# Performance work log

Measured on AMD Instinct MI355X. Metric: run time of the kernel, lower is better.

The kernel has to match this reference:

```python
import jax, jax.numpy as jnp
import numpy as np
import math

B, M, N = 1, 128, 256
LIG_C = 256      # rep_1d num_c
ATTN_C = 32      # attention_num_c
HEADS = 8        # num_heads
EPS = 1e-5


def setup_inputs() -> dict:
    key = jax.random.key(0)
    ks = jax.random.split(key, 8)
    s = 1.0 / math.sqrt(LIG_C)
    return {
        "lig_profile": jax.random.normal(ks[0], (B, M, N, LIG_C), dtype=jnp.float32),
        "ln_scale": jnp.ones((LIG_C,), dtype=jnp.float32),
        "ln_bias": jnp.zeros((LIG_C,), dtype=jnp.float32),
        "wq": jax.random.normal(ks[1], (LIG_C, ATTN_C * HEADS), dtype=jnp.float32) * s,
        "wk": jax.random.normal(ks[2], (LIG_C, ATTN_C * HEADS), dtype=jnp.float32) * s,
        "wv": jax.random.normal(ks[3], (LIG_C, ATTN_C * HEADS), dtype=jnp.float32) * s,
        "wf": jax.random.normal(ks[4], (ATTN_C * HEADS, LIG_C), dtype=jnp.float32) * s,
        "bf": jnp.zeros((LIG_C,), dtype=jnp.float32),
    }


def reference(lig_profile, ln_scale, ln_bias, wq, wk, wv, wf, bf):
    # LayerNorm over channel dim
    mu = jnp.mean(lig_profile, axis=-1, keepdims=True)
    var = jnp.mean(jnp.square(lig_profile - mu), axis=-1, keepdims=True)
    x = (lig_profile - mu) * jax.lax.rsqrt(var + EPS) * ln_scale + ln_bias

    # QKV projections; view splits last dim as (attn_c, heads) -> channel-major layout
    shape5 = x.shape[:-1] + (ATTN_C, HEADS)
    q = (x @ wq).reshape(shape5)  # [b,m,n,c,h]
    k = (x @ wk).reshape(shape5)
    v = (x @ wv).reshape(shape5)

    factor = 1.0 / math.sqrt(ATTN_C)
    aff = jnp.einsum('bmich,bmjch->bmijh', q, k) * factor  # [b,m,i,j,h]
    weights = jax.nn.softmax(aff, axis=-2)                  # softmax over j (keys)
    out = jnp.einsum('bmrch,bmirh->bmich', v, weights)      # [b,m,i,c,h]
    out = out.reshape(out.shape[:-2] + (ATTN_C * HEADS,))
    return out @ wf + bf
```

## Files before the change

kernel.cpp:

```cpp
#include <hip/hip_runtime.h>

typedef _Float16 f16;
typedef _Float16 f16x8 __attribute__((ext_vector_type(8)));
typedef _Float16 f16x4 __attribute__((ext_vector_type(4)));
typedef _Float16 f16x2 __attribute__((ext_vector_type(2)));
typedef float f32x4 __attribute__((ext_vector_type(4)));
typedef float f32x16 __attribute__((ext_vector_type(16)));

#define MDIM 128
#define NDIM 256
#define CDIM 256
#define ROWS (MDIM*NDIM)
#define L2E 1.4426950408889634f

__device__ inline int pk2(float a, float b) {
  union { f16x2 h; int i; } u;
  u.h[0] = (f16)a; u.h[1] = (f16)b;
  return u.i;
}

__global__ __launch_bounds__(256) void k_prep(
    const float* __restrict__ wq, const float* __restrict__ wk,
    const float* __restrict__ wv, const float* __restrict__ wf,
    f16* __restrict__ bq, f16* __restrict__ bk, f16* __restrict__ bv,
    f16* __restrict__ bw)
{
  __shared__ f16 ld[16][264];
  int which = blockIdx.x >> 4, kb = blockIdx.x & 15;
  int t = threadIdx.x;
  int k0 = kb * 16;
  if (which < 3) {
    const float* W = which == 0 ? wq : which == 1 ? wk : wv;
    f16* dst       = which == 0 ? bq : which == 1 ? bk : bv;
    float sc = which == 0 ? 0.17677669529663689f : 1.0f;
#pragma unroll
    for (int r = 0; r < 16; ++r)
      ld[r][t] = (f16)(W[(size_t)(k0 + r) * 256 + t] * sc);
    __syncthreads();
    int j = (t & 31) * 8 + (t >> 5);
    f16x8 o;
#pragma unroll
    for (int i = 0; i < 8; ++i) o[i] = ld[i][j];
    *(f16x8*)(dst + (size_t)t * 256 + k0) = o;
#pragma unroll
    for (int i = 0; i < 8; ++i) o[i] = ld[8 + i][j];
    *(f16x8*)(dst + (size_t)t * 256 + k0 + 8) = o;
  } else {
#pragma unroll
    for (int r = 0; r < 16; ++r) {
      int ke = k0 + r;
      int jr = (ke & 31) * 8 + (ke >> 5);
      ld[r][t] = (f16)wf[(size_t)jr * 256 + t];
    }
    __syncthreads();
    f16x8 o;
#pragma unroll
    for (int i = 0; i < 8; ++i) o[i] = ld[i][t];
    *(f16x8*)(bw + (size_t)t * 256 + k0) = o;
#pragma unroll
    for (int i = 0; i < 8; ++i) o[i] = ld[8 + i][t];
    *(f16x8*)(bw + (size_t)t * 256 + k0 + 8) = o;
  }
}

__global__ __launch_bounds__(256) void k_ln(const float* __restrict__ x,
                                            const float* __restrict__ g,
                                            const float* __restrict__ b,
                                            f16* __restrict__ y)
{
  int row  = blockIdx.x * 4 + (threadIdx.x >> 6);
  int lane = threadIdx.x & 63;
  const float4 xv = *(const float4*)(x + (size_t)row * CDIM + lane * 4);
  float s  = xv.x + xv.y + xv.z + xv.w;
  float s2 = xv.x*xv.x + xv.y*xv.y + xv.z*xv.z + xv.w*xv.w;
#pragma unroll
  for (int m = 1; m < 64; m <<= 1) {
    s  += __shfl_xor(s,  m, 64);
    s2 += __shfl_xor(s2, m, 64);
  }
  float mu  = s * (1.0f / CDIM);
  float var = s2 * (1.0f / CDIM) - mu * mu;
  float rs  = rsqrtf(var + 1e-5f);
  const float4 gv = *(const float4*)(g + lane * 4);
  const float4 bv = *(const float4*)(b + lane * 4);
  f16x4 o;
  o[0] = (f16)((xv.x - mu) * rs * gv.x + bv.x);
  o[1] = (f16)((xv.y - mu) * rs * gv.y + bv.y);
  o[2] = (f16)((xv.z - mu) * rs * gv.z + bv.z);
  o[3] = (f16)((xv.w - mu) * rs * gv.w + bv.w);
  *(f16x4*)(y + (size_t)row * CDIM + lane * 4) = o;
}

__global__ __launch_bounds__(256) void k_qkv(const f16* __restrict__ xh,
    const f16* __restrict__ bq, const f16* __restrict__ bk, const f16* __restrict__ bv,
    f16* __restrict__ qo, f16* __restrict__ ko, f16* __restrict__ vT)
{
  __shared__ f16 Bs[64][264];
  __shared__ f16 vtmp[4][64][18];
  int mp = blockIdx.x;
  int nc = blockIdx.y;
  int sec = nc >> 2;
  int c0  = (nc & 3) * 64;
  const f16* B = sec == 0 ? bq : sec == 1 ? bk : bv;
  f16* dst     = sec == 0 ? qo : ko;
  int t = threadIdx.x, lane = t & 63, w = t >> 6;
  int l15 = lane & 15, l4 = lane >> 4;
  {
    int pr = t >> 2, pc = (t & 3) * 8;
#pragma unroll
    for (int p = 0; p < 8; ++p)
      *(f16x8*)&Bs[pr][pc + p * 32] =
        *(const f16x8*)(B + (size_t)(c0 + pr) * 256 + pc + p * 32);
  }
  __syncthreads();
  for (int it = 0; it < 4; ++it) {
    int r0 = mp * 256 + it * 64 + w * 16;
    f16x8 af[8];
#pragma unroll
    for (int kt = 0; kt < 8; ++kt)
      af[kt] = *(const f16x8*)(xh + (size_t)(r0 + l15) * 256 + kt * 32 + l4 * 8);
    f32x4 acc[4] = {};
#pragma unroll
    for (int kt = 0; kt < 8; ++kt) {
#pragma unroll
      for (int ni = 0; ni < 4; ++ni) {
        f16x8 bf = *(const f16x8*)&Bs[ni * 16 + l15][kt * 32 + l4 * 8];
        acc[ni] = __builtin_amdgcn_mfma_f32_16x16x32_f16(af[kt], bf, acc[ni], 0, 0, 0);
      }
    }
    if (sec < 2) {
#pragma unroll
      for (int ni = 0; ni < 4; ++ni)
#pragma unroll
        for (int r = 0; r < 4; ++r)
          dst[(size_t)(r0 + l4 * 4 + r) * 256 + c0 + ni * 16 + l15] = (f16)acc[ni][r];
    } else {
#pragma unroll
      for (int ni = 0; ni < 4; ++ni)
#pragma unroll
        for (int r = 0; r < 4; ++r)
          vtmp[w][ni * 16 + l15][l4 * 4 + r] = (f16)acc[ni][r];
      int n0 = it * 64 + w * 16;
      f16x8 v0 = *(const f16x8*)&vtmp[w][lane][0];
      f16x8 v1 = *(const f16x8*)&vtmp[w][lane][8];
      size_t gd = ((size_t)mp * 256 + c0 + lane) * 256 + n0;
      *(f16x8*)(vT + gd)     = v0;
      *(f16x8*)(vT + gd + 8) = v1;
    }
  }
}

__global__ __launch_bounds__(512, 4) void k_attn(const f16* __restrict__ q,
    const f16* __restrict__ k, const f16* __restrict__ vT, f16* __restrict__ o)
{
  __shared__ f16 ks[256][40];
  __shared__ f16 vt[32][264];
  int bx = blockIdx.x;
  int m = bx >> 3, h = bx & 7;
  int t = threadIdx.x, lane = t & 63, w = t >> 6;
  int i32 = lane & 31, hi = lane >> 5;
  size_t rowbase = (size_t)m * 256;
#pragma unroll
  for (int p = 0; p < 2; ++p) {
    int n = p * 128 + (t >> 2);
    int c0 = (t & 3) * 8;
    *(f16x8*)&ks[n][c0] = *(const f16x8*)(k + (rowbase + n) * 256 + h * 32 + c0);
  }
#pragma unroll
  for (int p = 0; p < 2; ++p) {
    int idx = p * 512 + t;
    int c = idx >> 5, nb = (idx & 31) * 8;
    *(f16x8*)&vt[c][nb] = *(const f16x8*)(vT + ((size_t)m * 256 + h * 32 + c) * 256 + nb);
  }
  __syncthreads();
  int qi0 = w * 32;
  const f16* qp = q + (rowbase + qi0 + i32) * 256 + h * 32 + hi * 8;
  f16x8 qf0 = *(const f16x8*)(qp);
  f16x8 qf1 = *(const f16x8*)(qp + 16);
  f32x16 O = {};
  float m_run = -1e30f, l_run = 0.f;
#pragma unroll 2
  for (int kb = 0; kb < 8; ++kb) {
    f16x8 kf0 = *(const f16x8*)&ks[kb * 32 + i32][hi * 8];
    f16x8 kf1 = *(const f16x8*)&ks[kb * 32 + i32][16 + hi * 8];
    f32x16 s = {};
    __builtin_amdgcn_s_setprio(1);
    s = __builtin_amdgcn_mfma_f32_32x32x16_f16(kf0, qf0, s, 0, 0, 0);
    s = __builtin_amdgcn_mfma_f32_32x32x16_f16(kf1, qf1, s, 0, 0, 0);
    __builtin_amdgcn_s_setprio(0);
#pragma unroll
    for (int r = 0; r < 16; ++r) s[r] *= L2E;
    float pmax = s[0];
#pragma unroll
    for (int r = 1; r < 16; ++r) pmax = fmaxf(pmax, s[r]);
    pmax = fmaxf(pmax, __shfl_xor(pmax, 32, 64));
    if (!__all(pmax - m_run <= 8.f)) {
      float m_new = fmaxf(m_run, pmax);
      float f = __builtin_amdgcn_exp2f(m_run - m_new);
      l_run *= f;
#pragma unroll
      for (int r = 0; r < 16; ++r)
        O[r] *= __shfl(f, (r & 3) + 8 * (r >> 2) + 4 * hi, 64);
      m_run = m_new;
    }
    float lsum = 0.f;
#pragma unroll
    for (int r = 0; r < 16; ++r) {
      float e = __builtin_amdgcn_exp2f(s[r] - m_run);
      s[r] = e;
      lsum += e;
    }
    lsum += __shfl_xor(lsum, 32, 64);
    l_run += lsum;
    int W0[4], W1[4];
#pragma unroll
    for (int qq = 0; qq < 4; ++qq) {
      W0[qq] = pk2(s[4 * qq],     s[4 * qq + 1]);
      W1[qq] = pk2(s[4 * qq + 2], s[4 * qq + 3]);
    }
#pragma unroll
    for (int ks2 = 0; ks2 < 2; ++ks2) {
      int X0 = W0[2 * ks2], Y0 = W0[2 * ks2 + 1];
      int X1 = W1[2 * ks2], Y1 = W1[2 * ks2 + 1];
      int a0 = __shfl(X0, i32, 64),      b0 = __shfl(Y0, i32, 64);
      int a1 = __shfl(X1, i32, 64),      b1 = __shfl(Y1, i32, 64);
      int a2 = __shfl(X0, i32 + 32, 64), b2 = __shfl(Y0, i32 + 32, 64);
      int a3 = __shfl(X1, i32 + 32, 64), b3 = __shfl(Y1, i32 + 32, 64);
      union { unsigned int ww[4]; f16x8 v; } pa;
      pa.ww[0] = hi ? (unsigned)b0 : (unsigned)a0;
      pa.ww[1] = hi ? (unsigned)b1 : (unsigned)a1;
      pa.ww[2] = hi ? (unsigned)b2 : (unsigned)a2;
      pa.ww[3] = hi ? (unsigned)b3 : (unsigned)a3;
      f16x8 vb = *(const f16x8*)&vt[i32][kb * 32 + ks2 * 16 + hi * 8];
      __builtin_amdgcn_s_setprio(1);
      O = __builtin_amdgcn_mfma_f32_32x32x16_f16(pa.v, vb, O, 0, 0, 0);
      __builtin_amdgcn_s_setprio(0);
    }
  }
  float inv = 1.f / l_run;
#pragma unroll
  for (int r = 0; r < 16; ++r) {
    int i = (r & 3) + 8 * (r >> 2) + 4 * hi;
    float fr = __shfl(inv, i, 64);
    o[(rowbase + (size_t)(qi0 + i)) * 256 + h * 32 + i32] = (f16)(O[r] * fr);
  }
}

__global__ __launch_bounds__(256) void k_out(const f16* __restrict__ a,
    const f16* __restrict__ bw, const float* __restrict__ bias,
    float* __restrict__ out)
{
  __shared__ f16 Bs[64][264];
  int mp = blockIdx.x;
  int nc = blockIdx.y;
  int c0 = nc * 64;
  int t = threadIdx.x, lane = t & 63, w = t >> 6;
  int l15 = lane & 15, l4 = lane >> 4;
  {
    int pr = t >> 2, pc = (t & 3) * 8;
#pragma unroll
    for (int p = 0; p < 8; ++p)
      *(f16x8*)&Bs[pr][pc + p * 32] =
        *(const f16x8*)(bw + (size_t)(c0 + pr) * 256 + pc + p * 32);
  }
  __syncthreads();
  float bv[4];
#pragma unroll
  for (int ni = 0; ni < 4; ++ni) bv[ni] = bias[c0 + ni * 16 + l15];
  for (int it = 0; it < 4; ++it) {
    int r0 = mp * 256 + it * 64 + w * 16;
    f16x8 af[8];
#pragma unroll
    for (int kt = 0; kt < 8; ++kt)
      af[kt] = *(const f16x8*)(a + (size_t)(r0 + l15) * 256 + kt * 32 + l4 * 8);
    f32x4 acc[4] = {};
#pragma unroll
    for (int kt = 0; kt < 8; ++kt) {
#pragma unroll
      for (int ni = 0; ni < 4; ++ni) {
        f16x8 bf = *(const f16x8*)&Bs[ni * 16 + l15][kt * 32 + l4 * 8];
        acc[ni] = __builtin_amdgcn_mfma_f32_16x16x32_f16(af[kt], bf, acc[ni], 0, 0, 0);
      }
    }
#pragma unroll
    for (int ni = 0; ni < 4; ++ni)
#pragma unroll
      for (int r = 0; r < 4; ++r)
        out[(size_t)(r0 + l4 * 4 + r) * 256 + c0 + ni * 16 + l15] = acc[ni][r] + bv[ni];
  }
}

extern "C" void kernel_launch(void* const* d_in, const int* in_sizes, int n_in,
                              void* d_out, int out_size, void* d_ws, size_t ws_size,
                              hipStream_t stream)
{
  const float* x  = (const float*)d_in[0];
  const float* g  = (const float*)d_in[1];
  const float* b  = (const float*)d_in[2];
  const float* wq = (const float*)d_in[3];
  const float* wk = (const float*)d_in[4];
  const float* wv = (const float*)d_in[5];
  const float* wf = (const float*)d_in[6];
  const float* bf = (const float*)d_in[7];
  float* out = (float*)d_out;

  char* ws = (char*)d_ws;
  f16* xh  = (f16*)(ws);
  f16* qh  = (f16*)(ws + (size_t)16 * 1024 * 1024);
  f16* kh  = (f16*)(ws + (size_t)32 * 1024 * 1024);
  f16* vTh = (f16*)(ws + (size_t)48 * 1024 * 1024);
  char* wbase = ws + (size_t)64 * 1024 * 1024;
  f16* bq = (f16*)(wbase);
  f16* bk = (f16*)(wbase + 128 * 1024);
  f16* bv = (f16*)(wbase + 256 * 1024);
  f16* bw = (f16*)(wbase + 384 * 1024);
  f16* ah = (f16*)(ws + (size_t)80 * 1024 * 1024);

  k_prep<<<64,            256, 0, stream>>>(wq, wk, wv, wf, bq, bk, bv, bw);
  k_ln  <<<ROWS / 4,      256, 0, stream>>>(x, g, b, xh);
  k_qkv <<<dim3(128, 12), 256, 0, stream>>>(xh, bq, bk, bv, qh, kh, vTh);
  k_attn<<<1024,          512, 0, stream>>>(qh, kh, vTh, ah);
  k_out <<<dim3(128, 4),  256, 0, stream>>>(ah, bw, bf, out);
}
```

Baseline: 95.07 us.

## Widen QKV tiles, drop V transpose, fold log2e into exp, retile output GEMM

The QKV GEMM now computes 128 output columns per block (6 column groups instead of 12) and writes V row-major, so the separate LDS transpose staging for V goes away. The attention kernel transposes V into shared memory itself with scalar LDS stores. It also folds the log2(e) scale into an FMA inside the exp and rescales the lazy-rescale threshold to match. The output GEMM is retiled so each block keeps a 64-row A tile in LDS and loops over four 64-column weight tiles, prefetching the next one into registers. The cost is scalar transposed LDS writes in attention, plus more loop iterations and barriers per block in the output GEMM.

```diff
diff --git a/kernel.cpp b/kernel.cpp
--- a/kernel.cpp
+++ b/kernel.cpp
@@ -93,24 +93,22 @@
 
 __global__ __launch_bounds__(256) void k_qkv(const f16* __restrict__ xh,
     const f16* __restrict__ bq, const f16* __restrict__ bk, const f16* __restrict__ bv,
-    f16* __restrict__ qo, f16* __restrict__ ko, f16* __restrict__ vT)
-{
-  __shared__ f16 Bs[64][264];
-  __shared__ f16 vtmp[4][64][18];
+    f16* __restrict__ qo, f16* __restrict__ ko, f16* __restrict__ vo)
+{
+  __shared__ f16 Bs[128][264];
   int mp = blockIdx.x;
   int nc = blockIdx.y;
-  int sec = nc >> 2;
-  int c0  = (nc & 3) * 64;
+  int sec = nc >> 1;
+  int c0  = (nc & 1) * 128;
   const f16* B = sec == 0 ? bq : sec == 1 ? bk : bv;
-  f16* dst     = sec == 0 ? qo : ko;
+  f16* dst     = sec == 0 ? qo : sec == 1 ? ko : vo;
   int t = threadIdx.x, lane = t & 63, w = t >> 6;
   int l15 = lane & 15, l4 = lane >> 4;
-  {
-    int pr = t >> 2, pc = (t & 3) * 8;
-#pragma unroll
-    for (int p = 0; p < 8; ++p)
-      *(f16x8*)&Bs[pr][pc + p * 32] =
-        *(const f16x8*)(B + (size_t)(c0 + pr) * 256 + pc + p * 32);
+#pragma unroll
+  for (int it = 0; it < 16; ++it) {
+    int id = it * 256 + t;
+    int br = id >> 5, bc = (id & 31) * 8;
+    *(f16x8*)&Bs[br][bc] = *(const f16x8*)(B + (size_t)(c0 + br) * 256 + bc);
   }
   __syncthreads();
   for (int it = 0; it < 4; ++it) {
@@ -119,39 +117,25 @@
 #pragma unroll
     for (int kt = 0; kt < 8; ++kt)
       af[kt] = *(const f16x8*)(xh + (size_t)(r0 + l15) * 256 + kt * 32 + l4 * 8);
-    f32x4 acc[4] = {};
+    f32x4 acc[8] = {};
 #pragma unroll
     for (int kt = 0; kt < 8; ++kt) {
 #pragma unroll
-      for (int ni = 0; ni < 4; ++ni) {
-        f16x8 bf = *(const f16x8*)&Bs[ni * 16 + l15][kt * 32 + l4 * 8];
-        acc[ni] = __builtin_amdgcn_mfma_f32_16x16x32_f16(af[kt], bf, acc[ni], 0, 0, 0);
+      for (int cf = 0; cf < 8; ++cf) {
+        f16x8 bf = *(const f16x8*)&Bs[cf * 16 + l15][kt * 32 + l4 * 8];
+        acc[cf] = __builtin_amdgcn_mfma_f32_16x16x32_f16(af[kt], bf, acc[cf], 0, 0, 0);
       }
     }
-    if (sec < 2) {
-#pragma unroll
-      for (int ni = 0; ni < 4; ++ni)
-#pragma unroll
-        for (int r = 0; r < 4; ++r)
-          dst[(size_t)(r0 + l4 * 4 + r) * 256 + c0 + ni * 16 + l15] = (f16)acc[ni][r];
-    } else {
-#pragma unroll
-      for (int ni = 0; ni < 4; ++ni)
-#pragma unroll
-        for (int r = 0; r < 4; ++r)
-          vtmp[w][ni * 16 + l15][l4 * 4 + r] = (f16)acc[ni][r];
-      int n0 = it * 64 + w * 16;
-      f16x8 v0 = *(const f16x8*)&vtmp[w][lane][0];
-      f16x8 v1 = *(const f16x8*)&vtmp[w][lane][8];
-      size_t gd = ((size_t)mp * 256 + c0 + lane) * 256 + n0;
-      *(f16x8*)(vT + gd)     = v0;
-      *(f16x8*)(vT + gd + 8) = v1;
-    }
+#pragma unroll
+    for (int cf = 0; cf < 8; ++cf)
+#pragma unroll
+      for (int r = 0; r < 4; ++r)
+        dst[(size_t)(r0 + l4 * 4 + r) * 256 + c0 + cf * 16 + l15] = (f16)acc[cf][r];
   }
 }
 
 __global__ __launch_bounds__(512, 4) void k_attn(const f16* __restrict__ q,
-    const f16* __restrict__ k, const f16* __restrict__ vT, f16* __restrict__ o)
+    const f16* __restrict__ k, const f16* __restrict__ v, f16* __restrict__ o)
 {
   __shared__ f16 ks[256][40];
   __shared__ f16 vt[32][264];
@@ -165,12 +149,9 @@
     int n = p * 128 + (t >> 2);
     int c0 = (t & 3) * 8;
     *(f16x8*)&ks[n][c0] = *(const f16x8*)(k + (rowbase + n) * 256 + h * 32 + c0);
-  }
-#pragma unroll
-  for (int p = 0; p < 2; ++p) {
-    int idx = p * 512 + t;
-    int c = idx >> 5, nb = (idx & 31) * 8;
-    *(f16x8*)&vt[c][nb] = *(const f16x8*)(vT + ((size_t)m * 256 + h * 32 + c) * 256 + nb);
+    f16x8 vv = *(const f16x8*)(v + (rowbase + n) * 256 + h * 32 + c0);
+#pragma unroll
+    for (int i = 0; i < 8; ++i) vt[c0 + i][n] = vv[i];
   }
   __syncthreads();
   int qi0 = w * 32;
@@ -178,7 +159,8 @@
   f16x8 qf0 = *(const f16x8*)(qp);
   f16x8 qf1 = *(const f16x8*)(qp + 16);
   f32x16 O = {};
-  float m_run = -1e30f, l_run = 0.f;
+  float m_run = -1e30f, l_run = 0.f, mL = -1e30f;
+  const float RTHR = 5.545177444479562f;
 #pragma unroll 2
   for (int kb = 0; kb < 8; ++kb) {
     f16x8 kf0 = *(const f16x8*)&ks[kb * 32 + i32][hi * 8];
@@ -188,25 +170,26 @@
     s = __builtin_amdgcn_mfma_f32_32x32x16_f16(kf0, qf0, s, 0, 0, 0);
     s = __builtin_amdgcn_mfma_f32_32x32x16_f16(kf1, qf1, s, 0, 0, 0);
     __builtin_amdgcn_s_setprio(0);
-#pragma unroll
-    for (int r = 0; r < 16; ++r) s[r] *= L2E;
-    float pmax = s[0];
-#pragma unroll
-    for (int r = 1; r < 16; ++r) pmax = fmaxf(pmax, s[r]);
+    float m0 = fmaxf(fmaxf(s[0], s[1]),  fmaxf(s[2], s[3]));
+    float m1 = fmaxf(fmaxf(s[4], s[5]),  fmaxf(s[6], s[7]));
+    float m2 = fmaxf(fmaxf(s[8], s[9]),  fmaxf(s[10], s[11]));
+    float m3 = fmaxf(fmaxf(s[12], s[13]), fmaxf(s[14], s[15]));
+    float pmax = fmaxf(fmaxf(m0, m1), fmaxf(m2, m3));
     pmax = fmaxf(pmax, __shfl_xor(pmax, 32, 64));
-    if (!__all(pmax - m_run <= 8.f)) {
+    if (!__all(pmax - m_run <= RTHR)) {
       float m_new = fmaxf(m_run, pmax);
-      float f = __builtin_amdgcn_exp2f(m_run - m_new);
+      float f = __builtin_amdgcn_exp2f((m_run - m_new) * L2E);
       l_run *= f;
 #pragma unroll
       for (int r = 0; r < 16; ++r)
         O[r] *= __shfl(f, (r & 3) + 8 * (r >> 2) + 4 * hi, 64);
       m_run = m_new;
+      mL = m_run * L2E;
     }
     float lsum = 0.f;
 #pragma unroll
     for (int r = 0; r < 16; ++r) {
-      float e = __builtin_amdgcn_exp2f(s[r] - m_run);
+      float e = __builtin_amdgcn_exp2f(__builtin_fmaf(s[r], L2E, -mL));
       s[r] = e;
       lsum += e;
     }
@@ -250,43 +233,54 @@
     const f16* __restrict__ bw, const float* __restrict__ bias,
     float* __restrict__ out)
 {
+  __shared__ f16 As[64][264];
   __shared__ f16 Bs[64][264];
-  int mp = blockIdx.x;
-  int nc = blockIdx.y;
-  int c0 = nc * 64;
+  int bm = blockIdx.x;
   int t = threadIdx.x, lane = t & 63, w = t >> 6;
+  int wr = w >> 1, wc = w & 1;
   int l15 = lane & 15, l4 = lane >> 4;
-  {
-    int pr = t >> 2, pc = (t & 3) * 8;
+  int pr = t >> 2, pc = (t & 3) * 8;
+  f16x8 pf[8];
+#pragma unroll
+  for (int p = 0; p < 8; ++p)
+    pf[p] = *(const f16x8*)(bw + (size_t)pr * 256 + pc + p * 32);
+#pragma unroll
+  for (int p = 0; p < 8; ++p)
+    *(f16x8*)&As[pr][pc + p * 32] = *(const f16x8*)(a + (size_t)(bm * 64 + pr) * 256 + pc + p * 32);
+  for (int ct = 0; ct < 4; ++ct) {
+    int col0 = ct * 64;
 #pragma unroll
     for (int p = 0; p < 8; ++p)
-      *(f16x8*)&Bs[pr][pc + p * 32] =
-        *(const f16x8*)(bw + (size_t)(c0 + pr) * 256 + pc + p * 32);
-  }
-  __syncthreads();
-  float bv[4];
-#pragma unroll
-  for (int ni = 0; ni < 4; ++ni) bv[ni] = bias[c0 + ni * 16 + l15];
-  for (int it = 0; it < 4; ++it) {
-    int r0 = mp * 256 + it * 64 + w * 16;
-    f16x8 af[8];
-#pragma unroll
-    for (int kt = 0; kt < 8; ++kt)
-      af[kt] = *(const f16x8*)(a + (size_t)(r0 + l15) * 256 + kt * 32 + l4 * 8);
-    f32x4 acc[4] = {};
+      *(f16x8*)&Bs[pr][pc + p * 32] = pf[p];
+    __syncthreads();
+    if (ct < 3) {
+#pragma unroll
+      for (int p = 0; p < 8; ++p)
+        pf[p] = *(const f16x8*)(bw + (size_t)((ct + 1) * 64 + pr) * 256 + pc + p * 32);
+    }
+    f32x4 acc[2][2] = {};
 #pragma unroll
     for (int kt = 0; kt < 8; ++kt) {
-#pragma unroll
-      for (int ni = 0; ni < 4; ++ni) {
-        f16x8 bf = *(const f16x8*)&Bs[ni * 16 + l15][kt * 32 + l4 * 8];
-        acc[ni] = __builtin_amdgcn_mfma_f32_16x16x32_f16(af[kt], bf, acc[ni], 0, 0, 0);
-      }
-    }
-#pragma unroll
-    for (int ni = 0; ni < 4; ++ni)
-#pragma unroll
-      for (int r = 0; r < 4; ++r)
-        out[(size_t)(r0 + l4 * 4 + r) * 256 + c0 + ni * 16 + l15] = acc[ni][r] + bv[ni];
+      f16x8 a0 = *(const f16x8*)&As[wr * 32 +      l15][kt * 32 + l4 * 8];
+      f16x8 a1 = *(const f16x8*)&As[wr * 32 + 16 + l15][kt * 32 + l4 * 8];
+      f16x8 b0 = *(const f16x8*)&Bs[wc * 32 +      l15][kt * 32 + l4 * 8];
+      f16x8 b1 = *(const f16x8*)&Bs[wc * 32 + 16 + l15][kt * 32 + l4 * 8];
+      acc[0][0] = __builtin_amdgcn_mfma_f32_16x16x32_f16(a0, b0, acc[0][0], 0, 0, 0);
+      acc[0][1] = __builtin_amdgcn_mfma_f32_16x16x32_f16(a0, b1, acc[0][1], 0, 0, 0);
+      acc[1][0] = __builtin_amdgcn_mfma_f32_16x16x32_f16(a1, b0, acc[1][0], 0, 0, 0);
+      acc[1][1] = __builtin_amdgcn_mfma_f32_16x16x32_f16(a1, b1, acc[1][1], 0, 0, 0);
+    }
+#pragma unroll
+    for (int mi = 0; mi < 2; ++mi)
+#pragma unroll
+      for (int ni = 0; ni < 2; ++ni)
+#pragma unroll
+        for (int r = 0; r < 4; ++r) {
+          int row = bm * 64 + wr * 32 + mi * 16 + l4 * 4 + r;
+          int col = col0 + wc * 32 + ni * 16 + l15;
+          out[(size_t)row * 256 + col] = acc[mi][ni][r] + bias[col];
+        }
+    __syncthreads();
   }
 }
 
@@ -308,7 +302,7 @@
   f16* xh  = (f16*)(ws);
   f16* qh  = (f16*)(ws + (size_t)16 * 1024 * 1024);
   f16* kh  = (f16*)(ws + (size_t)32 * 1024 * 1024);
-  f16* vTh = (f16*)(ws + (size_t)48 * 1024 * 1024);
+  f16* vh  = (f16*)(ws + (size_t)48 * 1024 * 1024);
   char* wbase = ws + (size_t)64 * 1024 * 1024;
   f16* bq = (f16*)(wbase);
   f16* bk = (f16*)(wbase + 128 * 1024);
@@ -316,9 +310,9 @@
   f16* bw = (f16*)(wbase + 384 * 1024);
   f16* ah = (f16*)(ws + (size_t)80 * 1024 * 1024);
 
-  k_prep<<<64,            256, 0, stream>>>(wq, wk, wv, wf, bq, bk, bv, bw);
-  k_ln  <<<ROWS / 4,      256, 0, stream>>>(x, g, b, xh);
-  k_qkv <<<dim3(128, 12), 256, 0, stream>>>(xh, bq, bk, bv, qh, kh, vTh);
-  k_attn<<<1024,          512, 0, stream>>>(qh, kh, vTh, ah);
-  k_out <<<dim3(128, 4),  256, 0, stream>>>(ah, bw, bf, out);
-}
+  k_prep<<<64,           256, 0, stream>>>(wq, wk, wv, wf, bq, bk, bv, bw);
+  k_ln  <<<ROWS / 4,     256, 0, stream>>>(x, g, b, xh);
+  k_qkv <<<dim3(128, 6), 256, 0, stream>>>(xh, bq, bk, bv, qh, kh, vh);
+  k_attn<<<1024,         512, 0, stream>>>(qh, kh, vh, ah);
+  k_out <<<512,          256, 0, stream>>>(ah, bw, bf, out);
+}
```

New measurement: 97.86 us. 2.9% more time.
